# Optimization experiments

Hardware: AMD Instinct MI355X
Metric: run time of the kernel (lower is better)

The kernel has to match this reference:

```python
import jax, jax.numpy as jnp
import numpy as np

N_NODES = 20000   # nodes per node type
N_CONTENT = 3     # content feature vectors per node
K_NBR = 10        # sampled neighbors per relation
DIM = 128
HID = DIM // 2    # 64, per-direction LSTM hidden


def _lstm_dir(x, Wih, Whh, b):
    """Single-direction LSTM (PyTorch gate order i,f,g,o). x:[N,T,D] -> hs:[N,T,H]."""
    xp = jnp.einsum('ntd,gd->ntg', x, Wih) + b  # precompute input projections [N,T,4H]
    H = Whh.shape[1]
    h0 = jnp.zeros((x.shape[0], H), x.dtype)

    def step(carry, xt):
        h, c = carry
        g = xt + h @ Whh.T
        i, f, gg, o = jnp.split(g, 4, axis=-1)
        c = jax.nn.sigmoid(f) * c + jax.nn.sigmoid(i) * jnp.tanh(gg)
        h = jax.nn.sigmoid(o) * jnp.tanh(c)
        return (h, c), h

    _, hs = jax.lax.scan(step, (h0, h0), jnp.swapaxes(xp, 0, 1))
    return jnp.swapaxes(hs, 0, 1)


def _bilstm_mean(x, Wih, Whh, b):
    """Bidirectional LSTM then mean over time. Wih:[2,4H,D], Whh:[2,4H,H], b:[2,4H]."""
    fwd = _lstm_dir(x, Wih[0], Whh[0], b[0])
    bwd = _lstm_dir(x[:, ::-1], Wih[1], Whh[1], b[1])[:, ::-1]
    return jnp.concatenate([fwd, bwd], axis=-1).mean(axis=1)  # [N, DIM]


def _hetgnn_forward(contents, nbrs, lstm_Wih, lstm_Whh, lstm_b, atten_w, atten_b):
    # C2: content encoding per node type (LSTM index 0..2)
    content_h = [_bilstm_mean(contents[i], lstm_Wih[i], lstm_Whh[i], lstm_b[i])
                 for i in range(3)]
    # C3: same-type neighbor aggregation; neighbor LSTM is per SOURCE type (index 3+s)
    neigh_h = [[_bilstm_mean(content_h[s][nbrs[d][s]],                # gather [N,K,DIM]
                             lstm_Wih[3 + s], lstm_Whh[3 + s], lstm_b[3 + s])
                for s in range(3)] for d in range(3)]
    # attention-weighted fusion of [neigh_a, neigh_p, neigh_v, self]
    out = []
    for n in range(3):
        d_h = content_h[n]                                  # [N, DIM]
        emb = jnp.stack(neigh_h[n] + [d_h], axis=1)         # [N, 4, DIM]
        pair = jnp.concatenate(
            [jnp.broadcast_to(d_h[:, None, :], emb.shape), emb], axis=-1)  # [N,4,2*DIM]
        score = jax.nn.leaky_relu(
            jnp.einsum('nkd,d->nk', pair, atten_w[n]) + atten_b[n])        # [N,4]
        attn = jax.nn.softmax(score, axis=1)
        out.append(jnp.einsum('nk,nkd->nd', attn, emb))
    return jnp.stack(out, axis=0)  # [3, N, DIM] ordered (a, p, v)


def setup_inputs() -> dict:
    key = jax.random.key(0)
    ks = jax.random.split(key, 24)
    d = {}
    for i, n in enumerate(['a', 'p', 'v']):
        d[f'content_{n}'] = jax.random.normal(ks[i], (N_NODES, N_CONTENT, DIM), jnp.float32)
    idx = 3
    for dt in ['a', 'p', 'v']:
        for st in ['a', 'p', 'v']:
            d[f'nbr_{dt}{st}'] = jax.random.randint(ks[idx], (N_NODES, K_NBR), 0, N_NODES)
            idx += 1
    s = 1.0 / np.sqrt(HID)
    d['lstm_Wih'] = jax.random.uniform(ks[12], (6, 2, 4 * HID, DIM), jnp.float32, -s, s)
    d['lstm_Whh'] = jax.random.uniform(ks[13], (6, 2, 4 * HID, HID), jnp.float32, -s, s)
    d['lstm_b'] = jax.random.uniform(ks[14], (6, 2, 4 * HID), jnp.float32, -s, s)
    d['atten_w'] = jax.random.normal(ks[15], (3, 2 * DIM), jnp.float32) * 0.05
    d['atten_b'] = jnp.zeros((3,), jnp.float32)
    return d


def reference(content_a, content_p, content_v,
              nbr_aa, nbr_ap, nbr_av, nbr_pa, nbr_pp, nbr_pv, nbr_va, nbr_vp, nbr_vv,
              lstm_Wih, lstm_Whh, lstm_b, atten_w, atten_b):
    contents = [content_a, content_p, content_v]
    nbrs = [[nbr_aa, nbr_ap, nbr_av],
            [nbr_pa, nbr_pp, nbr_pv],
            [nbr_va, nbr_vp, nbr_vv]]
    return _hetgnn_forward(contents, nbrs, lstm_Wih, lstm_Whh, lstm_b, atten_w, atten_b)
```

## Files before the change

### kernel.cpp

```cpp
#include <hip/hip_runtime.h>

#define NN 20000

typedef __attribute__((ext_vector_type(8))) short frag8;
typedef __attribute__((ext_vector_type(4))) float f32x4;

struct NbrPtrs { const int* p[9]; };
struct Cont3  { const float* c[3]; };

__device__ inline float bf2f(unsigned short u){ union{unsigned i; float f;} v; v.i=(unsigned)u<<16; return v.f; }
__device__ inline unsigned short f2bf(float f){ union{float f; unsigned i;} v; v.f=f;
  return (unsigned short)((v.i + 0x7fffu + ((v.i>>16)&1u)) >> 16); }
__device__ inline float sigm(float x){ return 1.f/(1.f+__expf(-x)); }
__device__ inline float tanh_(float x){ return 1.f - 2.f/(__expf(2.f*x)+1.f); }

__global__ void pack_kernel(const float* __restrict__ Wih, const float* __restrict__ Whh,
                            const float* __restrict__ bsrc,
                            unsigned short* __restrict__ WihF, unsigned short* __restrict__ WhhF,
                            float* __restrict__ biasF)
{
  const int NW = 12*32768, NH2 = 12*16384, NB = 12*256;
  const int total = NW + NH2 + NB;
  for (int i = blockIdx.x*blockDim.x + threadIdx.x; i < total; i += gridDim.x*blockDim.x) {
    if (i < NW) {
      int LD=i>>15, r=i&32767;
      int j=r&7, u=(r>>3)&63, m=(r>>9)&3, g=(r>>11)&3, kk=(r>>13)&3;
      WihF[i] = f2bf(Wih[((long)LD*256 + g*64+u)*128 + kk*32+m*8+j]);
    } else if (i < NW+NH2) {
      int e=i-NW, LD=e>>14, r=e&16383;
      int j=r&7, u=(r>>3)&63, m=(r>>9)&3, g=(r>>11)&3, kk=(r>>13)&1;
      WhhF[e] = f2bf(Whh[((long)LD*256 + g*64+u)*64 + kk*32+m*8+j]);
    } else {
      int e=i-NW-NH2;
      biasF[e] = bsrc[e];
    }
  }
}

template<int T, int ISC3>
__global__ __launch_bounds__(256, 2) void lstm_kernel(
    Cont3 xf, const unsigned short* __restrict__ xb,
    NbrPtrs nb, int dtype,
    const unsigned short* __restrict__ WihF, const unsigned short* __restrict__ WhhF,
    const float* __restrict__ biasF, unsigned short* __restrict__ outH)
{
  const int y = blockIdx.y, dir = y & 1, s = y >> 1;
  const int L = ISC3 ? 3 + s : s;
  const int* nbr = ISC3 ? nb.p[dtype*3 + s] : nullptr;
  const unsigned short* xbase16 = ISC3 ? xb + (long)s*NN*128 : nullptr;
  const float* xbase32 = ISC3 ? nullptr : xf.c[s];
  unsigned short* outp = outH + (long)s*NN*128;
  const int lane = threadIdx.x & 63, w = threadIdx.x >> 6;
  const int m = lane >> 4, q = lane & 15;
  const int LD = L*2 + dir;

  const unsigned short* wp = WihF + (long)LD*32768;
  const unsigned short* hp = WhhF + (long)LD*16384;
  frag8 Bp[4][4], Br[2][4];
#pragma unroll
  for (int kk=0;kk<4;kk++)
#pragma unroll
    for (int g=0;g<4;g++)
      Bp[kk][g] = *(const frag8*)(wp + ((((kk*4+g)*4 + m)*64) + w*16 + q)*8);
#pragma unroll
  for (int kk=0;kk<2;kk++)
#pragma unroll
    for (int g=0;g<4;g++)
      Br[kk][g] = *(const frag8*)(hp + ((((kk*4+g)*4 + m)*64) + w*16 + q)*8);
  float bias[4];
#pragma unroll
  for (int g=0;g<4;g++) bias[g] = biasF[LD*256 + g*64 + w*16 + q];

  __shared__ __align__(16) unsigned short Hlds[1024];

  for (int tile = blockIdx.x; tile < NN/16; tile += gridDim.x) {
    const int node0 = tile*16;
    ((uint2*)Hlds)[threadIdx.x] = make_uint2(0u,0u);
    __syncthreads();
    f32x4 cst = {0.f,0.f,0.f,0.f}, hsum = {0.f,0.f,0.f,0.f};
    for (int t=0; t<T; t++) {
      const int tt = dir ? (T-1-t) : t;
      frag8 Xf[4];
      if (ISC3) {
        int idx = nbr[(node0+q)*10 + tt];
        const unsigned short* xr = xbase16 + (long)idx*128;
#pragma unroll
        for (int kk=0;kk<4;kk++) Xf[kk] = *(const frag8*)(xr + kk*32 + m*8);
      } else {
        const float* xr = xbase32 + ((long)(node0+q)*3 + tt)*128;
#pragma unroll
        for (int kk=0;kk<4;kk++) {
          float4 f0 = *(const float4*)(xr + kk*32 + m*8);
          float4 f1 = *(const float4*)(xr + kk*32 + m*8 + 4);
          frag8 xv;
          xv[0]=(short)f2bf(f0.x); xv[1]=(short)f2bf(f0.y); xv[2]=(short)f2bf(f0.z); xv[3]=(short)f2bf(f0.w);
          xv[4]=(short)f2bf(f1.x); xv[5]=(short)f2bf(f1.y); xv[6]=(short)f2bf(f1.z); xv[7]=(short)f2bf(f1.w);
          Xf[kk] = xv;
        }
      }
      f32x4 acc[4];
#pragma unroll
      for (int g=0;g<4;g++) acc[g] = (f32x4){bias[g],bias[g],bias[g],bias[g]};
#pragma unroll
      for (int kk=0;kk<4;kk++)
#pragma unroll
        for (int g=0;g<4;g++)
          acc[g] = __builtin_amdgcn_mfma_f32_16x16x32_bf16(Xf[kk], Bp[kk][g], acc[g], 0,0,0);
#pragma unroll
      for (int kk=0;kk<2;kk++) {
        frag8 Ah = *(const frag8*)((const char*)Hlds + (q*128 + ((kk*64 + m*16) ^ ((q&7)<<4))));
#pragma unroll
        for (int g=0;g<4;g++)
          acc[g] = __builtin_amdgcn_mfma_f32_16x16x32_bf16(Ah, Br[kk][g], acc[g], 0,0,0);
      }
      __syncthreads();
#pragma unroll
      for (int r=0;r<4;r++) {
        float gi = sigm(acc[0][r]);
        float gf = sigm(acc[1][r]);
        float gg = tanh_(acc[2][r]);
        float go = sigm(acc[3][r]);
        float cc = gf*cst[r] + gi*gg;
        cst[r] = cc;
        float h = go*tanh_(cc);
        hsum[r] += h;
        int row = m*4 + r;
        int u = w*16 + q;
        *(unsigned short*)((char*)Hlds + (row*128 + ((2*u) ^ ((row&7)<<4)))) = f2bf(h);
      }
      __syncthreads();
    }
#pragma unroll
    for (int r=0;r<4;r++) {
      int node = node0 + m*4 + r;
      outp[(long)node*128 + dir*64 + w*16 + q] = f2bf(hsum[r]*(1.f/T));
    }
  }
}

__global__ __launch_bounds__(256) void attn_kernel(
    const unsigned short* __restrict__ ch, const unsigned short* __restrict__ nh,
    const float* __restrict__ awd, const float* __restrict__ ab, int d,
    float* __restrict__ outp)
{
  int i = blockIdx.x*4 + (threadIdx.x >> 6);
  if (i >= NN) return;
  int lane = threadIdx.x & 63;
  const float2 wlo = *(const float2*)(awd + 2*lane);
  const float2 whi = *(const float2*)(awd + 128 + 2*lane);
  unsigned sv = *(const unsigned*)(ch + (long)i*128 + 2*lane);
  float sx = bf2f((unsigned short)sv), sy = bf2f((unsigned short)(sv>>16));
  float ex[3], ey[3];
#pragma unroll
  for (int k=0;k<3;k++) {
    unsigned v = *(const unsigned*)(nh + ((long)k*NN + i)*128 + 2*lane);
    ex[k]=bf2f((unsigned short)v); ey[k]=bf2f((unsigned short)(v>>16));
  }
  float pd = sx*wlo.x + sy*wlo.y;
  float p[4];
#pragma unroll
  for (int k=0;k<3;k++) p[k] = ex[k]*whi.x + ey[k]*whi.y;
  p[3] = sx*whi.x + sy*whi.y;
#pragma unroll
  for (int off=1; off<64; off<<=1) {
    pd  += __shfl_xor(pd , off, 64);
    p[0]+= __shfl_xor(p[0],off, 64);
    p[1]+= __shfl_xor(p[1],off, 64);
    p[2]+= __shfl_xor(p[2],off, 64);
    p[3]+= __shfl_xor(p[3],off, 64);
  }
  float b = ab[d];
  float sc[4], mx=-1e30f;
#pragma unroll
  for (int k=0;k<4;k++){ float v = pd + p[k] + b; sc[k] = v>0.f ? v : 0.01f*v; mx = fmaxf(mx, sc[k]); }
  float es=0.f;
#pragma unroll
  for (int k=0;k<4;k++){ sc[k]=__expf(sc[k]-mx); es+=sc[k]; }
  float inv = 1.f/es;
  float ox = (sc[0]*ex[0]+sc[1]*ex[1]+sc[2]*ex[2]+sc[3]*sx)*inv;
  float oy = (sc[0]*ey[0]+sc[1]*ey[1]+sc[2]*ey[2]+sc[3]*sy)*inv;
  *(float2*)(outp + (long)i*128 + 2*lane) = make_float2(ox, oy);
}

extern "C" void kernel_launch(void* const* d_in, const int* in_sizes, int n_in,
                              void* d_out, int out_size, void* d_ws, size_t ws_size,
                              hipStream_t stream)
{
  Cont3 cc;
  cc.c[0] = (const float*)d_in[0];
  cc.c[1] = (const float*)d_in[1];
  cc.c[2] = (const float*)d_in[2];
  NbrPtrs nb;
  for (int k=0;k<9;k++) nb.p[k] = (const int*)d_in[3+k];
  const float* Wih = (const float*)d_in[12];
  const float* Whh = (const float*)d_in[13];
  const float* bb  = (const float*)d_in[14];
  const float* aw  = (const float*)d_in[15];
  const float* ab  = (const float*)d_in[16];

  char* wsp = (char*)d_ws;
  unsigned short* WihF = (unsigned short*)wsp;     wsp += 786432;
  unsigned short* WhhF = (unsigned short*)wsp;     wsp += 393216;
  float* biasF = (float*)wsp;                      wsp += 12288;
  unsigned short* contentH = (unsigned short*)wsp; wsp += 15360000;
  unsigned short* scratch  = (unsigned short*)wsp;

  pack_kernel<<<1024, 256, 0, stream>>>(Wih, Whh, bb, WihF, WhhF, biasF);
  lstm_kernel<3,0><<<dim3(250,6), 256, 0, stream>>>(cc, nullptr, nb, 0, WihF, WhhF, biasF, contentH);
  for (int d=0; d<3; d++) {
    lstm_kernel<10,1><<<dim3(250,6), 256, 0, stream>>>(cc, contentH, nb, d, WihF, WhhF, biasF, scratch);
    attn_kernel<<<NN/4, 256, 0, stream>>>(contentH + (long)d*NN*128, scratch,
                                          aw + d*256, ab, d,
                                          (float*)d_out + (long)d*NN*128);
  }
}
```

Measured before the change: 1.080 ms.

## Rewrite LSTM kernel with prefetch, fused bias-exp2 gates, and merged launches

Rewrites the LSTM kernel. The next timestep's input fragments are now double-buffered and prefetched, the h state is ping-ponged in LDS so each step needs one barrier instead of two, and the bias is folded into exp2-based sigmoid/tanh using rcp intrinsics with bf16 packing via v_cvt_pk. Weights are repacked into a per-wave fragment layout and staged through LDS. The three per-destination neighbor LSTM launches and attention launches are each merged into single larger grids, and occupancy launch bounds are relaxed. This cuts barrier stalls, transcendental cost and launch overhead, but uses more registers and LDS and approximate rcp/exp.

```diff
diff --git a/kernel.cpp b/kernel.cpp
--- a/kernel.cpp
+++ b/kernel.cpp
@@ -1,6 +1,7 @@
 #include <hip/hip_runtime.h>
 
 #define NN 20000
+#define LOG2E 1.44269504088896f
 
 typedef __attribute__((ext_vector_type(8))) short frag8;
 typedef __attribute__((ext_vector_type(4))) float f32x4;
@@ -11,149 +12,194 @@
 __device__ inline float bf2f(unsigned short u){ union{unsigned i; float f;} v; v.i=(unsigned)u<<16; return v.f; }
 __device__ inline unsigned short f2bf(float f){ union{float f; unsigned i;} v; v.f=f;
   return (unsigned short)((v.i + 0x7fffu + ((v.i>>16)&1u)) >> 16); }
-__device__ inline float sigm(float x){ return 1.f/(1.f+__expf(-x)); }
-__device__ inline float tanh_(float x){ return 1.f - 2.f/(__expf(2.f*x)+1.f); }
+__device__ inline unsigned cvtpk(float a, float b){ unsigned r;
+  asm("v_cvt_pk_bf16_f32 %0, %1, %2" : "=v"(r) : "v"(a), "v"(b)); return r; }
 
 __global__ void pack_kernel(const float* __restrict__ Wih, const float* __restrict__ Whh,
                             const float* __restrict__ bsrc,
-                            unsigned short* __restrict__ WihF, unsigned short* __restrict__ WhhF,
-                            float* __restrict__ biasF)
-{
-  const int NW = 12*32768, NH2 = 12*16384, NB = 12*256;
-  const int total = NW + NH2 + NB;
-  for (int i = blockIdx.x*blockDim.x + threadIdx.x; i < total; i += gridDim.x*blockDim.x) {
-    if (i < NW) {
-      int LD=i>>15, r=i&32767;
-      int j=r&7, u=(r>>3)&63, m=(r>>9)&3, g=(r>>11)&3, kk=(r>>13)&3;
-      WihF[i] = f2bf(Wih[((long)LD*256 + g*64+u)*128 + kk*32+m*8+j]);
-    } else if (i < NW+NH2) {
-      int e=i-NW, LD=e>>14, r=e&16383;
-      int j=r&7, u=(r>>3)&63, m=(r>>9)&3, g=(r>>11)&3, kk=(r>>13)&1;
-      WhhF[e] = f2bf(Whh[((long)LD*256 + g*64+u)*64 + kk*32+m*8+j]);
+                            unsigned short* __restrict__ WF, float* __restrict__ biasB)
+{
+  const int NWF = 589824, NB = 3072;
+  for (int e = blockIdx.x*blockDim.x + threadIdx.x; e < NWF+NB; e += gridDim.x*blockDim.x) {
+    if (e < NWF) {
+      int t = e >> 9, r = e & 511;
+      int lane = r >> 3, j = r & 7;
+      int fi = t % 24, s2 = t / 24;
+      int w = s2 & 3, LD = s2 >> 2;
+      int m = lane >> 4, q = lane & 15;
+      float v;
+      if (fi < 16) {
+        int kk = fi >> 2, g = fi & 3;
+        v = Wih[((long)LD*256 + g*64 + w*16 + q)*128 + kk*32 + m*8 + j];
+      } else {
+        int f2 = fi - 16, kk = f2 >> 2, g = f2 & 3;
+        v = Whh[((long)LD*256 + g*64 + w*16 + q)*64 + kk*32 + m*8 + j];
+      }
+      WF[e] = f2bf(v);
     } else {
-      int e=i-NW-NH2;
-      biasF[e] = bsrc[e];
-    }
-  }
+      int e2 = e - NWF;
+      int g = (e2 >> 6) & 3;
+      float b = bsrc[e2];
+      biasB[e2] = (g==2) ? b*(2.f*LOG2E) : -b*LOG2E;
+    }
+  }
+}
+
+__device__ inline frag8 load_x_f32(const float* xr, int off){
+  float4 f0 = *(const float4*)(xr + off);
+  float4 f1 = *(const float4*)(xr + off + 4);
+  union { frag8 f; unsigned u[4]; } r;
+  r.u[0]=cvtpk(f0.x,f0.y); r.u[1]=cvtpk(f0.z,f0.w);
+  r.u[2]=cvtpk(f1.x,f1.y); r.u[3]=cvtpk(f1.z,f1.w);
+  return r.f;
 }
 
 template<int T, int ISC3>
-__global__ __launch_bounds__(256, 2) void lstm_kernel(
-    Cont3 xf, const unsigned short* __restrict__ xb,
-    NbrPtrs nb, int dtype,
-    const unsigned short* __restrict__ WihF, const unsigned short* __restrict__ WhhF,
-    const float* __restrict__ biasF, unsigned short* __restrict__ outH)
-{
-  const int y = blockIdx.y, dir = y & 1, s = y >> 1;
-  const int L = ISC3 ? 3 + s : s;
-  const int* nbr = ISC3 ? nb.p[dtype*3 + s] : nullptr;
-  const unsigned short* xbase16 = ISC3 ? xb + (long)s*NN*128 : nullptr;
-  const float* xbase32 = ISC3 ? nullptr : xf.c[s];
-  unsigned short* outp = outH + (long)s*NN*128;
-  const int lane = threadIdx.x & 63, w = threadIdx.x >> 6;
+__global__ __launch_bounds__(256) void lstm2(
+    Cont3 xf, const unsigned short* __restrict__ xb, NbrPtrs nb,
+    const unsigned short* __restrict__ WF, const float* __restrict__ biasB,
+    unsigned short* __restrict__ outH)
+{
+  const int y = blockIdx.y, dir = y & 1, sl = y >> 1;
+  const int s = ISC3 ? (sl % 3) : sl;
+  const int LD = (ISC3 ? 3 + s : s)*2 + dir;
+  const int* nbr = ISC3 ? nb.p[sl] : nullptr;
+  const unsigned short* xb16 = ISC3 ? xb + (long)s*NN*128 : nullptr;
+  const float* xb32 = ISC3 ? nullptr : xf.c[s];
+  unsigned short* outp = outH + (long)sl*NN*128;
+
+  const int tid = threadIdx.x, lane = tid & 63, w = tid >> 6;
   const int m = lane >> 4, q = lane & 15;
-  const int LD = L*2 + dir;
-
-  const unsigned short* wp = WihF + (long)LD*32768;
-  const unsigned short* hp = WhhF + (long)LD*16384;
+
+  __shared__ __align__(16) char lds[24576];
+
   frag8 Bp[4][4], Br[2][4];
-#pragma unroll
-  for (int kk=0;kk<4;kk++)
-#pragma unroll
-    for (int g=0;g<4;g++)
-      Bp[kk][g] = *(const frag8*)(wp + ((((kk*4+g)*4 + m)*64) + w*16 + q)*8);
-#pragma unroll
-  for (int kk=0;kk<2;kk++)
-#pragma unroll
-    for (int g=0;g<4;g++)
-      Br[kk][g] = *(const frag8*)(hp + ((((kk*4+g)*4 + m)*64) + w*16 + q)*8);
-  float bias[4];
-#pragma unroll
-  for (int g=0;g<4;g++) bias[g] = biasF[LD*256 + g*64 + w*16 + q];
-
-  __shared__ __align__(16) unsigned short Hlds[1024];
+  for (int rr = 0; rr < 4; rr++) {
+    const uint4* src = (const uint4*)(WF + ((long)(LD*4 + rr)*24)*512);
+#pragma unroll
+    for (int it = 0; it < 6; it++)
+      ((uint4*)lds)[tid + it*256] = src[tid + it*256];
+    __syncthreads();
+    if (w == rr) {
+#pragma unroll
+      for (int fi = 0; fi < 16; fi++)
+        Bp[fi>>2][fi&3] = *(const frag8*)(lds + fi*1024 + lane*16);
+#pragma unroll
+      for (int fi = 16; fi < 24; fi++)
+        Br[(fi-16)>>2][(fi-16)&3] = *(const frag8*)(lds + fi*1024 + lane*16);
+    }
+    __syncthreads();
+  }
+  const float bI = biasB[LD*256 +   0 + w*16 + q];
+  const float bF = biasB[LD*256 +  64 + w*16 + q];
+  const float bG = biasB[LD*256 + 128 + w*16 + q];
+  const float bO = biasB[LD*256 + 192 + w*16 + q];
+
+  int rd[2][2], wra[2][4];
+#pragma unroll
+  for (int kk=0;kk<2;kk++){
+    int o = q*128 + ((kk*64 + m*16) ^ ((q&7)<<4));
+    rd[0][kk]=o; rd[1][kk]=o+2048;
+  }
+#pragma unroll
+  for (int r=0;r<4;r++){
+    int row = m*4 + r, uu = w*16 + q;
+    int o = row*128 + ((2*uu) ^ ((row&7)<<4));
+    wra[0][r]=o; wra[1][r]=o+2048;
+  }
+  const int u = w*16 + q;
+  const f32x4 Z = {0.f,0.f,0.f,0.f};
 
   for (int tile = blockIdx.x; tile < NN/16; tile += gridDim.x) {
     const int node0 = tile*16;
-    ((uint2*)Hlds)[threadIdx.x] = make_uint2(0u,0u);
-    __syncthreads();
-    f32x4 cst = {0.f,0.f,0.f,0.f}, hsum = {0.f,0.f,0.f,0.f};
+    f32x4 cst = {0,0,0,0}, hsum = {0,0,0,0};
+    frag8 X[2][4];
+    {
+      const int tt0 = dir ? (T-1) : 0;
+      if (ISC3) {
+        int idx = nbr[(node0+q)*10 + tt0];
+        const unsigned short* xr = xb16 + (long)idx*128;
+#pragma unroll
+        for (int kk=0;kk<4;kk++) X[0][kk] = *(const frag8*)(xr + kk*32 + m*8);
+      } else {
+        const float* xr = xb32 + ((long)(node0+q)*3 + tt0)*128;
+#pragma unroll
+        for (int kk=0;kk<4;kk++) X[0][kk] = load_x_f32(xr, kk*32 + m*8);
+      }
+    }
+#pragma unroll
     for (int t=0; t<T; t++) {
-      const int tt = dir ? (T-1-t) : t;
-      frag8 Xf[4];
-      if (ISC3) {
-        int idx = nbr[(node0+q)*10 + tt];
-        const unsigned short* xr = xbase16 + (long)idx*128;
-#pragma unroll
-        for (int kk=0;kk<4;kk++) Xf[kk] = *(const frag8*)(xr + kk*32 + m*8);
-      } else {
-        const float* xr = xbase32 + ((long)(node0+q)*3 + tt)*128;
-#pragma unroll
-        for (int kk=0;kk<4;kk++) {
-          float4 f0 = *(const float4*)(xr + kk*32 + m*8);
-          float4 f1 = *(const float4*)(xr + kk*32 + m*8 + 4);
-          frag8 xv;
-          xv[0]=(short)f2bf(f0.x); xv[1]=(short)f2bf(f0.y); xv[2]=(short)f2bf(f0.z); xv[3]=(short)f2bf(f0.w);
-          xv[4]=(short)f2bf(f1.x); xv[5]=(short)f2bf(f1.y); xv[6]=(short)f2bf(f1.z); xv[7]=(short)f2bf(f1.w);
-          Xf[kk] = xv;
+      const int cb = t & 1, nb2 = cb ^ 1;
+      f32x4 acc[4];
+#pragma unroll
+      for (int g=0;g<4;g++)
+        acc[g] = __builtin_amdgcn_mfma_f32_16x16x32_bf16(X[cb][0], Bp[0][g], Z, 0,0,0);
+#pragma unroll
+      for (int kk=1;kk<4;kk++)
+#pragma unroll
+        for (int g=0;g<4;g++)
+          acc[g] = __builtin_amdgcn_mfma_f32_16x16x32_bf16(X[cb][kk], Bp[kk][g], acc[g], 0,0,0);
+      if (t > 0) {
+#pragma unroll
+        for (int kk=0;kk<2;kk++) {
+          frag8 Ah = *(const frag8*)(lds + rd[cb][kk]);
+#pragma unroll
+          for (int g=0;g<4;g++)
+            acc[g] = __builtin_amdgcn_mfma_f32_16x16x32_bf16(Ah, Br[kk][g], acc[g], 0,0,0);
         }
       }
-      f32x4 acc[4];
-#pragma unroll
-      for (int g=0;g<4;g++) acc[g] = (f32x4){bias[g],bias[g],bias[g],bias[g]};
-#pragma unroll
-      for (int kk=0;kk<4;kk++)
-#pragma unroll
-        for (int g=0;g<4;g++)
-          acc[g] = __builtin_amdgcn_mfma_f32_16x16x32_bf16(Xf[kk], Bp[kk][g], acc[g], 0,0,0);
-#pragma unroll
-      for (int kk=0;kk<2;kk++) {
-        frag8 Ah = *(const frag8*)((const char*)Hlds + (q*128 + ((kk*64 + m*16) ^ ((q&7)<<4))));
-#pragma unroll
-        for (int g=0;g<4;g++)
-          acc[g] = __builtin_amdgcn_mfma_f32_16x16x32_bf16(Ah, Br[kk][g], acc[g], 0,0,0);
-      }
-      __syncthreads();
+      if (t+1 < T) {
+        const int tt = dir ? (T-2-t) : (t+1);
+        if (ISC3) {
+          int idx = nbr[(node0+q)*10 + tt];
+          const unsigned short* xr = xb16 + (long)idx*128;
+#pragma unroll
+          for (int kk=0;kk<4;kk++) X[nb2][kk] = *(const frag8*)(xr + kk*32 + m*8);
+        } else {
+          const float* xr = xb32 + ((long)(node0+q)*3 + tt)*128;
+#pragma unroll
+          for (int kk=0;kk<4;kk++) X[nb2][kk] = load_x_f32(xr, kk*32 + m*8);
+        }
+      }
 #pragma unroll
       for (int r=0;r<4;r++) {
-        float gi = sigm(acc[0][r]);
-        float gf = sigm(acc[1][r]);
-        float gg = tanh_(acc[2][r]);
-        float go = sigm(acc[3][r]);
-        float cc = gf*cst[r] + gi*gg;
+        float gi = __builtin_amdgcn_rcpf(1.f + __builtin_amdgcn_exp2f(fmaf(acc[0][r], -LOG2E, bI)));
+        float gf = __builtin_amdgcn_rcpf(1.f + __builtin_amdgcn_exp2f(fmaf(acc[1][r], -LOG2E, bF)));
+        float tg = fmaf(-2.f, __builtin_amdgcn_rcpf(1.f + __builtin_amdgcn_exp2f(fmaf(acc[2][r], 2.f*LOG2E, bG))), 1.f);
+        float go = __builtin_amdgcn_rcpf(1.f + __builtin_amdgcn_exp2f(fmaf(acc[3][r], -LOG2E, bO)));
+        float cc = fmaf(gf, cst[r], gi*tg);
         cst[r] = cc;
-        float h = go*tanh_(cc);
+        float tc = fmaf(-2.f, __builtin_amdgcn_rcpf(1.f + __builtin_amdgcn_exp2f(cc*(2.f*LOG2E))), 1.f);
+        float h = go*tc;
         hsum[r] += h;
-        int row = m*4 + r;
-        int u = w*16 + q;
-        *(unsigned short*)((char*)Hlds + (row*128 + ((2*u) ^ ((row&7)<<4)))) = f2bf(h);
+        *(unsigned short*)(lds + wra[nb2][r]) = (unsigned short)cvtpk(h, h);
       }
       __syncthreads();
     }
 #pragma unroll
     for (int r=0;r<4;r++) {
       int node = node0 + m*4 + r;
-      outp[(long)node*128 + dir*64 + w*16 + q] = f2bf(hsum[r]*(1.f/T));
+      outp[(long)node*128 + dir*64 + u] = f2bf(hsum[r]*(1.f/T));
     }
   }
 }
 
 __global__ __launch_bounds__(256) void attn_kernel(
     const unsigned short* __restrict__ ch, const unsigned short* __restrict__ nh,
-    const float* __restrict__ awd, const float* __restrict__ ab, int d,
-    float* __restrict__ outp)
-{
-  int i = blockIdx.x*4 + (threadIdx.x >> 6);
-  if (i >= NN) return;
+    const float* __restrict__ aw, const float* __restrict__ ab,
+    float* __restrict__ out)
+{
+  int wid = blockIdx.x*4 + (threadIdx.x >> 6);
+  int n = wid / NN, i = wid - n*NN;
   int lane = threadIdx.x & 63;
-  const float2 wlo = *(const float2*)(awd + 2*lane);
-  const float2 whi = *(const float2*)(awd + 128 + 2*lane);
-  unsigned sv = *(const unsigned*)(ch + (long)i*128 + 2*lane);
+  const float2 wlo = *(const float2*)(aw + n*256 + 2*lane);
+  const float2 whi = *(const float2*)(aw + n*256 + 128 + 2*lane);
+  unsigned sv = *(const unsigned*)(ch + ((long)n*NN + i)*128 + 2*lane);
   float sx = bf2f((unsigned short)sv), sy = bf2f((unsigned short)(sv>>16));
   float ex[3], ey[3];
 #pragma unroll
   for (int k=0;k<3;k++) {
-    unsigned v = *(const unsigned*)(nh + ((long)k*NN + i)*128 + 2*lane);
+    unsigned v = *(const unsigned*)(nh + ((long)(n*3+k)*NN + i)*128 + 2*lane);
     ex[k]=bf2f((unsigned short)v); ey[k]=bf2f((unsigned short)(v>>16));
   }
   float pd = sx*wlo.x + sy*wlo.y;
@@ -169,7 +215,7 @@
     p[2]+= __shfl_xor(p[2],off, 64);
     p[3]+= __shfl_xor(p[3],off, 64);
   }
-  float b = ab[d];
+  float b = ab[n];
   float sc[4], mx=-1e30f;
 #pragma unroll
   for (int k=0;k<4;k++){ float v = pd + p[k] + b; sc[k] = v>0.f ? v : 0.01f*v; mx = fmaxf(mx, sc[k]); }
@@ -179,7 +225,7 @@
   float inv = 1.f/es;
   float ox = (sc[0]*ex[0]+sc[1]*ex[1]+sc[2]*ex[2]+sc[3]*sx)*inv;
   float oy = (sc[0]*ey[0]+sc[1]*ey[1]+sc[2]*ey[2]+sc[3]*sy)*inv;
-  *(float2*)(outp + (long)i*128 + 2*lane) = make_float2(ox, oy);
+  *(float2*)(out + ((long)n*NN + i)*128 + 2*lane) = make_float2(ox, oy);
 }
 
 extern "C" void kernel_launch(void* const* d_in, const int* in_sizes, int n_in,
@@ -199,18 +245,13 @@
   const float* ab  = (const float*)d_in[16];
 
   char* wsp = (char*)d_ws;
-  unsigned short* WihF = (unsigned short*)wsp;     wsp += 786432;
-  unsigned short* WhhF = (unsigned short*)wsp;     wsp += 393216;
-  float* biasF = (float*)wsp;                      wsp += 12288;
-  unsigned short* contentH = (unsigned short*)wsp; wsp += 15360000;
-  unsigned short* scratch  = (unsigned short*)wsp;
-
-  pack_kernel<<<1024, 256, 0, stream>>>(Wih, Whh, bb, WihF, WhhF, biasF);
-  lstm_kernel<3,0><<<dim3(250,6), 256, 0, stream>>>(cc, nullptr, nb, 0, WihF, WhhF, biasF, contentH);
-  for (int d=0; d<3; d++) {
-    lstm_kernel<10,1><<<dim3(250,6), 256, 0, stream>>>(cc, contentH, nb, d, WihF, WhhF, biasF, scratch);
-    attn_kernel<<<NN/4, 256, 0, stream>>>(contentH + (long)d*NN*128, scratch,
-                                          aw + d*256, ab, d,
-                                          (float*)d_out + (long)d*NN*128);
-  }
-}
+  unsigned short* WF = (unsigned short*)wsp;        wsp += 1179648;
+  float* biasB = (float*)wsp;                       wsp += 12288;
+  unsigned short* contentH = (unsigned short*)wsp;  wsp += 15360000;
+  unsigned short* neighH   = (unsigned short*)wsp;
+
+  pack_kernel<<<1024, 256, 0, stream>>>(Wih, Whh, bb, WF, biasB);
+  lstm2<3,0><<<dim3(625,6),  256, 0, stream>>>(cc, nullptr,  nb, WF, biasB, contentH);
+  lstm2<10,1><<<dim3(625,18),256, 0, stream>>>(cc, contentH, nb, WF, biasB, neighH);
+  attn_kernel<<<(3*NN)/4, 256, 0, stream>>>(contentH, neighH, aw, ab, (float*)d_out);
+}
```

Measured after the change: 954.2 us. 1.13x faster.
